# Kernel tuning notes

Hardware: AMD Instinct MI355X
Metric: run time of the kernel (lower is better)

The kernel has to match this reference:

```python
import jax, jax.numpy as jnp
import numpy as np

B, N, M, D = 4, 2048, 2048, 512
BLUR, SCALING, P = 0.05, 0.9, 2          # geomloss: blur=epsilon, p=2
DIAMETER = 2.0                            # max distance between unit-norm points
# geomloss epsilon_schedule: diameter^p annealed down to blur^p by scaling^p
_sched = np.arange(P * np.log(DIAMETER), P * np.log(BLUR), P * np.log(SCALING))
EPS_LIST = np.concatenate([[DIAMETER ** P], np.exp(_sched), [BLUR ** P]]).astype(np.float32)


def setup_inputs() -> dict:
    key = jax.random.key(0)
    k1, k2 = jax.random.split(key)
    return {
        "E_p": jax.random.normal(k1, (B, N, D), jnp.float32),
        "E_t": jax.random.normal(k2, (B, M, D), jnp.float32),
    }


def _l2norm(x):
    return x / jnp.maximum(jnp.linalg.norm(x, axis=-1, keepdims=True), 1e-12)


def _cost(x, y):
    # C(x,y) = ||x - y||^2 / 2  (geomloss squared_distances / 2 for p=2)
    x2 = jnp.sum(x * x, axis=-1)[:, :, None]   # (B, N, 1)
    y2 = jnp.sum(y * y, axis=-1)[:, None, :]   # (B, 1, M)
    return 0.5 * (x2 + y2 - 2.0 * jnp.einsum("bnd,bmd->bnm", x, y))


def _softmin(eps, C, h):
    # h: (B, M) = log_weights + potential/eps ;  returns (B, N)
    return -eps * jax.nn.logsumexp(h[:, None, :] - C / eps, axis=-1)


def _sinkhorn_divergence(x, y):
    b, n = x.shape[0], x.shape[1]
    m = y.shape[1]
    C_xy = _cost(x, y)
    C_yx = jnp.swapaxes(C_xy, 1, 2)
    C_xx = _cost(x, x)
    C_yy = _cost(y, y)
    log_a = jnp.full((b, n), -np.log(n), x.dtype)   # uniform weights
    log_b = jnp.full((b, m), -np.log(m), x.dtype)

    sg = jax.lax.stop_gradient
    Cxy_s, Cyx_s, Cxx_s, Cyy_s = sg(C_xy), sg(C_yx), sg(C_xx), sg(C_yy)

    # init at the largest epsilon (geomloss sinkhorn_loop init)
    eps0 = float(EPS_LIST[0])
    f_ba = _softmin(eps0, Cxy_s, log_b)
    g_ab = _softmin(eps0, Cyx_s, log_a)
    f_aa = _softmin(eps0, Cxx_s, log_a)
    g_bb = _softmin(eps0, Cyy_s, log_b)

    def body(carry, eps):
        f_aa, g_bb, g_ab, f_ba = carry
        ft_ba = _softmin(eps, Cxy_s, log_b + g_ab / eps)
        gt_ab = _softmin(eps, Cyx_s, log_a + f_ba / eps)
        ft_aa = _softmin(eps, Cxx_s, log_a + f_aa / eps)
        gt_bb = _softmin(eps, Cyy_s, log_b + g_bb / eps)
        new = (0.5 * (f_aa + ft_aa), 0.5 * (g_bb + gt_bb),
               0.5 * (g_ab + gt_ab), 0.5 * (f_ba + ft_ba))
        return new, None

    (f_aa, g_bb, g_ab, f_ba), _ = jax.lax.scan(
        body, (f_aa, g_bb, g_ab, f_ba), jnp.asarray(EPS_LIST))

    # last extrapolation at final eps (gradients flow through the cost only,
    # matching geomloss's detached-potential final step)
    eps = float(EPS_LIST[-1])
    f_ba_f = _softmin(eps, C_xy, sg(log_b + g_ab / eps))
    g_ab_f = _softmin(eps, C_yx, sg(log_a + f_ba / eps))
    f_aa_f = _softmin(eps, C_xx, sg(log_a + f_aa / eps))
    g_bb_f = _softmin(eps, C_yy, sg(log_b + g_bb / eps))

    a_w = jnp.exp(log_a)
    b_w = jnp.exp(log_b)
    loss = (jnp.sum(a_w * (f_ba_f - f_aa_f), axis=-1)
            + jnp.sum(b_w * (g_ab_f - g_bb_f), axis=-1))   # (B,)
    return jnp.mean(loss)


def reference(E_p, E_t):
    return _sinkhorn_divergence(_l2norm(E_p), _l2norm(E_t))
```

## Files before the change

### kernel.cpp

```cpp
#include <hip/hip_runtime.h>
#include <hip/hip_bf16.h>
#include <hip/hip_fp16.h>
#include <math.h>

#define B_ 4
#define N_ 2048
#define D_ 512

typedef __bf16    bf16x8  __attribute__((ext_vector_type(8)));
typedef float     floatx4 __attribute__((ext_vector_type(4)));
typedef _Float16  half8   __attribute__((ext_vector_type(8)));

#if __has_builtin(__builtin_amdgcn_exp2f)
__device__ __forceinline__ float fexp2(float x) { return __builtin_amdgcn_exp2f(x); }
#else
__device__ __forceinline__ float fexp2(float x) { return exp2f(x); }
#endif
#if __has_builtin(__builtin_amdgcn_logf)
__device__ __forceinline__ float flog2(float x) { return __builtin_amdgcn_logf(x); }
#else
__device__ __forceinline__ float flog2(float x) { return __log2f(x); }
#endif

__device__ __forceinline__ void gload16(const void* g, void* l) {
  __builtin_amdgcn_global_load_lds(
      (const __attribute__((address_space(1))) void*)g,
      (__attribute__((address_space(3))) void*)l, 16, 0, 0);
}

__global__ __launch_bounds__(256) void norm_kernel(const float* __restrict__ in,
                                                   __hip_bfloat16* __restrict__ out) {
  const size_t row = blockIdx.x;
  const int t = threadIdx.x;
  const float* src = in + row * D_;
  float v0 = src[t], v1 = src[t + 256];
  float ss = fmaf(v0, v0, v1 * v1);
#pragma unroll
  for (int off = 1; off < 64; off <<= 1) ss += __shfl_xor(ss, off);
  __shared__ float red[4];
  if ((t & 63) == 0) red[t >> 6] = ss;
  __syncthreads();
  const float tot = red[0] + red[1] + red[2] + red[3];
  const float scale = 1.0f / fmaxf(sqrtf(tot), 1e-12f);
  out[row * D_ + t]       = __float2bfloat16(v0 * scale);
  out[row * D_ + t + 256] = __float2bfloat16(v1 * scale);
}

__global__ __launch_bounds__(256) void gram_gemm(const __hip_bfloat16* __restrict__ X,
                                                 const __hip_bfloat16* __restrict__ Y,
                                                 __half* __restrict__ Gxy,
                                                 __half* __restrict__ Gxx,
                                                 __half* __restrict__ Gyy) {
  __shared__ __hip_bfloat16 As[128 * 32];
  __shared__ __hip_bfloat16 Bs[128 * 32];
  const int t = threadIdx.x;
  const int wave = t >> 6, lane = t & 63;
  const int bm0 = blockIdx.x * 128, bn0 = blockIdx.y * 128;
  const int mat = blockIdx.z >> 2;
  const size_t bb = blockIdx.z & 3;
  const __hip_bfloat16* Ab = (mat == 2 ? Y : X) + bb * (size_t)(N_ * D_);
  const __hip_bfloat16* Bb = (mat == 1 ? X : Y) + bb * (size_t)(N_ * D_);
  __half* Gb = (mat == 0 ? Gxy : mat == 1 ? Gxx : Gyy) + bb * (size_t)N_ * N_;

  floatx4 acc[4][4] = {};
  const int wr = wave >> 1, wc = wave & 1;
  const int srow = t >> 2;
  const int scol = (t & 3) * 8;
  char* AsB = (char*)As;
  char* BsB = (char*)Bs;
  const int ldsOff = wave * 1024;

  for (int k0 = 0; k0 < D_; k0 += 32) {
    __syncthreads();
    gload16(Ab + (size_t)(bm0 + srow)      * D_ + k0 + scol, AsB + ldsOff);
    gload16(Ab + (size_t)(bm0 + 64 + srow) * D_ + k0 + scol, AsB + 4096 + ldsOff);
    gload16(Bb + (size_t)(bn0 + srow)      * D_ + k0 + scol, BsB + ldsOff);
    gload16(Bb + (size_t)(bn0 + 64 + srow) * D_ + k0 + scol, BsB + 4096 + ldsOff);
    __syncthreads();

    const int lrow = lane & 15, lk = (lane >> 4) * 8;
    bf16x8 af[4], bfr[4];
#pragma unroll
    for (int mi = 0; mi < 4; ++mi)
      af[mi] = *(const bf16x8*)((const char*)As + ((wr * 64 + mi * 16 + lrow) * 32 + lk) * 2);
#pragma unroll
    for (int ni = 0; ni < 4; ++ni)
      bfr[ni] = *(const bf16x8*)((const char*)Bs + ((wc * 64 + ni * 16 + lrow) * 32 + lk) * 2);
#pragma unroll
    for (int mi = 0; mi < 4; ++mi)
#pragma unroll
      for (int ni = 0; ni < 4; ++ni)
        acc[mi][ni] = __builtin_amdgcn_mfma_f32_16x16x32_bf16(af[mi], bfr[ni], acc[mi][ni], 0, 0, 0);
  }

  const int orow = (lane >> 4) * 4, ocol = lane & 15;
#pragma unroll
  for (int mi = 0; mi < 4; ++mi)
#pragma unroll
    for (int ni = 0; ni < 4; ++ni) {
      const int row = bm0 + wr * 64 + mi * 16 + orow;
      const int col = bn0 + wc * 64 + ni * 16 + ocol;
#pragma unroll
      for (int r = 0; r < 4; ++r)
        Gb[(size_t)(row + r) * N_ + col] = __float2half(acc[mi][ni][r]);
    }
}

#define L2E_ 1.44269504088896f
#define LN2_ 0.69314718055995f

template <int MODE>
__global__ __launch_bounds__(256) void sink_stream(
    const __half* __restrict__ Gxy, const __half* __restrict__ Gxx,
    const __half* __restrict__ Gyy,
    const float* __restrict__ potOld, float* __restrict__ potNew,
    float2* __restrict__ colPart, float eps, float* __restrict__ out) {
  __shared__ float2 part[4][32];

  const int bid = blockIdx.x;
  const int mat = bid % 3;
  const int rem = bid / 3;
  const int b = rem >> 6, stripe = rem & 63;
  const int lane = threadIdx.x & 63, wave = threadIdx.x >> 6;
  const int c0 = wave * 512 + lane * 8;

  const float inv_eps = 1.0f / eps;
  const float ieL  = inv_eps * L2E_;
  const float hbL  = (-7.62461898616f - inv_eps) * L2E_;
  const float negEpsLn2 = -eps * LN2_;

  const __half* G = (mat == 0 ? Gxy : mat == 1 ? Gxx : Gyy) + (size_t)b * N_ * N_;
  const int hIdx = (mat == 0) ? 1 : (mat == 1) ? 2 : 3;
  const int oIdx = (mat == 0) ? 0 : hIdx;
  const float* potH = potOld + ((size_t)hIdx * B_ + b) * N_;
  const float* potR = potOld + ((size_t)0    * B_ + b) * N_;
  const float* potO = potOld + ((size_t)oIdx * B_ + b) * N_;
  float*       potW = potNew + ((size_t)oIdx * B_ + b) * N_;

  float hh[8];
  if constexpr (MODE == 0) {
#pragma unroll
    for (int e = 0; e < 8; ++e) hh[e] = hbL;
  } else {
    const float4 a = *(const float4*)(potH + c0);
    const float4 c = *(const float4*)(potH + c0 + 4);
    hh[0] = fmaf(a.x, ieL, hbL); hh[1] = fmaf(a.y, ieL, hbL);
    hh[2] = fmaf(a.z, ieL, hbL); hh[3] = fmaf(a.w, ieL, hbL);
    hh[4] = fmaf(c.x, ieL, hbL); hh[5] = fmaf(c.y, ieL, hbL);
    hh[6] = fmaf(c.z, ieL, hbL); hh[7] = fmaf(c.w, ieL, hbL);
  }

  float colm[8], cols_[8];
#pragma unroll
  for (int e = 0; e < 8; ++e) { colm[e] = -3.0e38f; cols_[e] = 0.0f; }

  const int rbase = stripe * 32;
  const __half* gbase = G + (size_t)rbase * N_ + c0;

  half8 A0, A1, P0, P1;
  A0 = *(const half8*)(gbase);
  A1 = *(const half8*)(gbase + N_);

#pragma unroll 1
  for (int it = 0; it < 16; ++it) {
    if (it < 15) {
      const __half* gp = gbase + (size_t)(it * 2 + 2) * N_;
      P0 = *(const half8*)(gp);
      P1 = *(const half8*)(gp + N_);
    }

    const int r0 = rbase + it * 2;
    float hr0 = hbL, hr1 = hbL;
    if (mat == 0 && MODE != 0) {
      hr0 = fmaf(potR[r0],     ieL, hbL);
      hr1 = fmaf(potR[r0 + 1], ieL, hbL);
    }

    float t0[8], t1[8];
    float mx0 = -3.0e38f, mx1 = -3.0e38f;
#pragma unroll
    for (int e = 0; e < 8; ++e) {
      t0[e] = fmaf((float)A0[e], ieL, hh[e]);
      t1[e] = fmaf((float)A1[e], ieL, hh[e]);
      mx0 = fmaxf(mx0, t0[e]);
      mx1 = fmaxf(mx1, t1[e]);
    }
#pragma unroll
    for (int off = 1; off < 64; off <<= 1) {
      mx0 = fmaxf(mx0, __shfl_xor(mx0, off));
      mx1 = fmaxf(mx1, __shfl_xor(mx1, off));
    }

    float sm0 = 0.0f, sm1 = 0.0f;
#pragma unroll
    for (int e = 0; e < 8; ++e) {
      sm0 += fexp2(t0[e] - mx0);
      sm1 += fexp2(t1[e] - mx1);
    }
#pragma unroll
    for (int off = 1; off < 64; off <<= 1) {
      sm0 += __shfl_xor(sm0, off);
      sm1 += __shfl_xor(sm1, off);
    }
    if (lane == 0) {
      part[wave][it * 2]     = make_float2(mx0, sm0);
      part[wave][it * 2 + 1] = make_float2(mx1, sm1);
    }

    if (mat == 0) {
      const float d0 = hr0, d1 = hr1;
#pragma unroll
      for (int e = 0; e < 8; ++e) {
        const float s0 = t0[e] - hh[e] + d0;
        const float s1 = t1[e] - hh[e] + d1;
        const float nm = fmaxf(colm[e], fmaxf(s0, s1));
        const float add = fexp2(s0 - nm) + fexp2(s1 - nm);
        cols_[e] = fmaf(cols_[e], fexp2(colm[e] - nm), add);
        colm[e] = nm;
      }
    }

    A0 = P0; A1 = P1;
  }

  if (mat == 0) {
    float2* cp = colPart + ((size_t)(b * 64 + stripe) * 2048 + c0);
#pragma unroll
    for (int e = 0; e < 8; ++e) cp[e] = make_float2(colm[e], cols_[e]);
  }

  __syncthreads();

  float vfin = 0.0f;
  if (wave == 0 && lane < 32) {
    float2 q = part[0][lane];
    float m = q.x, s = q.y;
#pragma unroll
    for (int w = 1; w < 4; ++w) {
      const float2 q2 = part[w][lane];
      const float nm = fmaxf(m, q2.x);
      s = fmaf(s, fexp2(m - nm), q2.y * fexp2(q2.x - nm));
      m = nm;
    }
    const float v = negEpsLn2 * (m + flog2(s));
    const int r = rbase + lane;
    if constexpr (MODE == 0) {
      potW[r] = v;
    } else if constexpr (MODE == 1) {
      potW[r] = 0.5f * (potO[r] + v);
    } else {
      vfin = v;
    }
  }

  if constexpr (MODE == 2) {
#pragma unroll
    for (int off = 1; off < 64; off <<= 1) vfin += __shfl_xor(vfin, off);
    if (threadIdx.x == 0) {
      const float sign = (mat == 0) ? 1.0f : -1.0f;
      atomicAdd(out, sign * vfin * (1.0f / (2048.0f * B_)));
    }
  }
}

template <int MODE>
__global__ __launch_bounds__(256) void sink_merge(
    const float2* __restrict__ colPart, const float* __restrict__ potOld,
    float* __restrict__ potNew, float eps, float* __restrict__ out) {
  __shared__ float2 mp[3][64];
  const int lane = threadIdx.x & 63, sub = threadIdx.x >> 6;
  const int colg = blockIdx.x * 64 + lane;
  const int b = colg >> 11, col = colg & 2047;
  const float negEpsLn2 = -eps * LN2_;

  float m = -3.0e38f, s = 0.0f;
  const float2* cp = colPart + ((size_t)(b * 64 + sub * 16)) * 2048 + col;
#pragma unroll
  for (int st = 0; st < 16; ++st) {
    const float2 P = cp[(size_t)st * 2048];
    const float nm = fmaxf(m, P.x);
    s = fmaf(s, fexp2(m - nm), P.y * fexp2(P.x - nm));
    m = nm;
  }
  if (sub != 0) mp[sub - 1][lane] = make_float2(m, s);
  __syncthreads();

  float vfin = 0.0f;
  if (sub == 0) {
#pragma unroll
    for (int w = 0; w < 3; ++w) {
      const float2 q = mp[w][lane];
      const float nm = fmaxf(m, q.x);
      s = fmaf(s, fexp2(m - nm), q.y * fexp2(q.x - nm));
      m = nm;
    }
    const float v = negEpsLn2 * (m + flog2(s));
    if constexpr (MODE == 0) {
      potNew[((size_t)1 * B_ + b) * N_ + col] = v;
    } else if constexpr (MODE == 1) {
      potNew[((size_t)1 * B_ + b) * N_ + col] =
          0.5f * (potOld[((size_t)1 * B_ + b) * N_ + col] + v);
    } else {
      vfin = v;
    }
  }

  if constexpr (MODE == 2) {
#pragma unroll
    for (int off = 1; off < 64; off <<= 1) vfin += __shfl_xor(vfin, off);
    __shared__ float red[4];
    if ((threadIdx.x & 63) == 0) red[sub] = vfin;
    __syncthreads();
    if (threadIdx.x == 0)
      atomicAdd(out, (red[0] + red[1] + red[2] + red[3]) * (1.0f / (2048.0f * B_)));
  }
}

extern "C" void kernel_launch(void* const* d_in, const int* in_sizes, int n_in,
                              void* d_out, int out_size, void* d_ws, size_t ws_size,
                              hipStream_t stream) {
  const float* E_p = (const float*)d_in[0];
  const float* E_t = (const float*)d_in[1];
  float* out = (float*)d_out;
  char* ws = (char*)d_ws;

  size_t off = 0;
  auto alloc = [&](size_t bytes) {
    void* p = ws + off;
    off += (bytes + 255) & ~(size_t)255;
    return p;
  };
  __hip_bfloat16* Xb = (__hip_bfloat16*)alloc((size_t)B_ * N_ * D_ * 2);
  __hip_bfloat16* Yb = (__hip_bfloat16*)alloc((size_t)B_ * N_ * D_ * 2);
  __half* Gxy = (__half*)alloc((size_t)B_ * N_ * N_ * 2);
  __half* Gxx = (__half*)alloc((size_t)B_ * N_ * N_ * 2);
  __half* Gyy = (__half*)alloc((size_t)B_ * N_ * N_ * 2);
  float* potA = (float*)alloc((size_t)4 * B_ * N_ * 4);
  float* potB = (float*)alloc((size_t)4 * B_ * N_ * 4);
  float2* colPart = (float2*)alloc((size_t)B_ * 64 * 2048 * 8);

  norm_kernel<<<B_ * N_, 256, 0, stream>>>(E_p, Xb);
  norm_kernel<<<B_ * N_, 256, 0, stream>>>(E_t, Yb);

  dim3 gg(16, 16, 12);
  gram_gemm<<<gg, 256, 0, stream>>>(Xb, Yb, Gxy, Gxx, Gyy);

  float epsl[48];
  int ne = 0;
  epsl[ne++] = 4.0f;
  {
    const double lstart = 2.0 * log(2.0);
    const double lstop  = 2.0 * log(0.05);
    const double lstep  = 2.0 * log(0.9);
    for (int k = 0;; ++k) {
      const double v = lstart + k * lstep;
      if (!(v > lstop)) break;
      epsl[ne++] = (float)exp(v);
    }
  }
  epsl[ne++] = 0.0025f;

  (void)hipMemsetAsync(d_out, 0, sizeof(float), stream);

  sink_stream<0><<<768, 256, 0, stream>>>(Gxy, Gxx, Gyy, potA, potA, colPart,
                                          epsl[0], nullptr);
  sink_merge<0><<<128, 256, 0, stream>>>(colPart, potA, potA, epsl[0], nullptr);

  float* cur = potA;
  float* nxt = potB;
  for (int i = 0; i < ne; ++i) {
    sink_stream<1><<<768, 256, 0, stream>>>(Gxy, Gxx, Gyy, cur, nxt, colPart,
                                            epsl[i], nullptr);
    sink_merge<1><<<128, 256, 0, stream>>>(colPart, cur, nxt, epsl[i], nullptr);
    float* tmp = cur; cur = nxt; nxt = tmp;
  }

  sink_stream<2><<<768, 256, 0, stream>>>(Gxy, Gxx, Gyy, cur, cur, colPart,
                                          epsl[ne - 1], out);
  sink_merge<2><<<128, 256, 0, stream>>>(colPart, cur, cur, epsl[ne - 1], out);
}
```

Before: 1.273 ms.

## Halve stripe height to double grid and process four rows per iteration

New measurement: 1.379 ms. 1.08x slower.

```diff
diff --git a/kernel.cpp b/kernel.cpp
--- a/kernel.cpp
+++ b/kernel.cpp
@@ -115,12 +115,12 @@
     const __half* __restrict__ Gyy,
     const float* __restrict__ potOld, float* __restrict__ potNew,
     float2* __restrict__ colPart, float eps, float* __restrict__ out) {
-  __shared__ float2 part[4][32];
+  __shared__ float2 part[4][16];
 
   const int bid = blockIdx.x;
   const int mat = bid % 3;
   const int rem = bid / 3;
-  const int b = rem >> 6, stripe = rem & 63;
+  const int b = rem >> 7, stripe = rem & 127;
   const int lane = threadIdx.x & 63, wave = threadIdx.x >> 6;
   const int c0 = wave * 512 + lane * 8;
 
@@ -154,77 +154,86 @@
 #pragma unroll
   for (int e = 0; e < 8; ++e) { colm[e] = -3.0e38f; cols_[e] = 0.0f; }
 
-  const int rbase = stripe * 32;
+  const int rbase = stripe * 16;
   const __half* gbase = G + (size_t)rbase * N_ + c0;
 
-  half8 A0, A1, P0, P1;
-  A0 = *(const half8*)(gbase);
-  A1 = *(const half8*)(gbase + N_);
+  half8 A[4], P[4];
+#pragma unroll
+  for (int r = 0; r < 4; ++r) A[r] = *(const half8*)(gbase + (size_t)r * N_);
 
 #pragma unroll 1
-  for (int it = 0; it < 16; ++it) {
-    if (it < 15) {
-      const __half* gp = gbase + (size_t)(it * 2 + 2) * N_;
-      P0 = *(const half8*)(gp);
-      P1 = *(const half8*)(gp + N_);
-    }
-
-    const int r0 = rbase + it * 2;
-    float hr0 = hbL, hr1 = hbL;
-    if (mat == 0 && MODE != 0) {
-      hr0 = fmaf(potR[r0],     ieL, hbL);
-      hr1 = fmaf(potR[r0 + 1], ieL, hbL);
-    }
-
-    float t0[8], t1[8];
-    float mx0 = -3.0e38f, mx1 = -3.0e38f;
-#pragma unroll
-    for (int e = 0; e < 8; ++e) {
-      t0[e] = fmaf((float)A0[e], ieL, hh[e]);
-      t1[e] = fmaf((float)A1[e], ieL, hh[e]);
-      mx0 = fmaxf(mx0, t0[e]);
-      mx1 = fmaxf(mx1, t1[e]);
+  for (int it = 0; it < 4; ++it) {
+    if (it < 3) {
+#pragma unroll
+      for (int r = 0; r < 4; ++r)
+        P[r] = *(const half8*)(gbase + (size_t)(it * 4 + 4 + r) * N_);
+    }
+
+    const int r0 = rbase + it * 4;
+    float hr[4];
+    if (mat == 0) {
+      if constexpr (MODE != 0) {
+#pragma unroll
+        for (int r = 0; r < 4; ++r) hr[r] = fmaf(potR[r0 + r], ieL, hbL);
+      } else {
+#pragma unroll
+        for (int r = 0; r < 4; ++r) hr[r] = hbL;
+      }
+    }
+
+    float mx[4];
+#pragma unroll
+    for (int r = 0; r < 4; ++r) {
+      float m = fmaf((float)A[r][0], ieL, hh[0]);
+#pragma unroll
+      for (int e = 1; e < 8; ++e) m = fmaxf(m, fmaf((float)A[r][e], ieL, hh[e]));
+      mx[r] = m;
     }
 #pragma unroll
     for (int off = 1; off < 64; off <<= 1) {
-      mx0 = fmaxf(mx0, __shfl_xor(mx0, off));
-      mx1 = fmaxf(mx1, __shfl_xor(mx1, off));
-    }
-
-    float sm0 = 0.0f, sm1 = 0.0f;
-#pragma unroll
-    for (int e = 0; e < 8; ++e) {
-      sm0 += fexp2(t0[e] - mx0);
-      sm1 += fexp2(t1[e] - mx1);
-    }
+#pragma unroll
+      for (int r = 0; r < 4; ++r) mx[r] = fmaxf(mx[r], __shfl_xor(mx[r], off));
+    }
+
+    float sm[4] = {0.0f, 0.0f, 0.0f, 0.0f};
+#pragma unroll
+    for (int r = 0; r < 4; ++r)
+#pragma unroll
+      for (int e = 0; e < 8; ++e)
+        sm[r] += fexp2(fmaf((float)A[r][e], ieL, hh[e]) - mx[r]);
 #pragma unroll
     for (int off = 1; off < 64; off <<= 1) {
-      sm0 += __shfl_xor(sm0, off);
-      sm1 += __shfl_xor(sm1, off);
-    }
+#pragma unroll
+      for (int r = 0; r < 4; ++r) sm[r] += __shfl_xor(sm[r], off);
+    }
+
     if (lane == 0) {
-      part[wave][it * 2]     = make_float2(mx0, sm0);
-      part[wave][it * 2 + 1] = make_float2(mx1, sm1);
+#pragma unroll
+      for (int r = 0; r < 4; ++r)
+        part[wave][it * 4 + r] = make_float2(mx[r], sm[r]);
     }
 
     if (mat == 0) {
-      const float d0 = hr0, d1 = hr1;
 #pragma unroll
       for (int e = 0; e < 8; ++e) {
-        const float s0 = t0[e] - hh[e] + d0;
-        const float s1 = t1[e] - hh[e] + d1;
-        const float nm = fmaxf(colm[e], fmaxf(s0, s1));
-        const float add = fexp2(s0 - nm) + fexp2(s1 - nm);
+        const float s0 = fmaf((float)A[0][e], ieL, hr[0]);
+        const float s1 = fmaf((float)A[1][e], ieL, hr[1]);
+        const float s2 = fmaf((float)A[2][e], ieL, hr[2]);
+        const float s3 = fmaf((float)A[3][e], ieL, hr[3]);
+        const float nm = fmaxf(fmaxf(fmaxf(s0, s1), fmaxf(s2, s3)), colm[e]);
+        const float add = fexp2(s0 - nm) + fexp2(s1 - nm)
+                        + fexp2(s2 - nm) + fexp2(s3 - nm);
         cols_[e] = fmaf(cols_[e], fexp2(colm[e] - nm), add);
         colm[e] = nm;
       }
     }
 
-    A0 = P0; A1 = P1;
+#pragma unroll
+    for (int r = 0; r < 4; ++r) A[r] = P[r];
   }
 
   if (mat == 0) {
-    float2* cp = colPart + ((size_t)(b * 64 + stripe) * 2048 + c0);
+    float2* cp = colPart + ((size_t)(b * 128 + stripe) * 2048 + c0);
 #pragma unroll
     for (int e = 0; e < 8; ++e) cp[e] = make_float2(colm[e], cols_[e]);
   }
@@ -232,7 +241,7 @@
   __syncthreads();
 
   float vfin = 0.0f;
-  if (wave == 0 && lane < 32) {
+  if (wave == 0 && lane < 16) {
     float2 q = part[0][lane];
     float m = q.x, s = q.y;
 #pragma unroll
@@ -274,9 +283,9 @@
   const float negEpsLn2 = -eps * LN2_;
 
   float m = -3.0e38f, s = 0.0f;
-  const float2* cp = colPart + ((size_t)(b * 64 + sub * 16)) * 2048 + col;
-#pragma unroll
-  for (int st = 0; st < 16; ++st) {
+  const float2* cp = colPart + ((size_t)(b * 128 + sub * 32)) * 2048 + col;
+#pragma unroll 8
+  for (int st = 0; st < 32; ++st) {
     const float2 P = cp[(size_t)st * 2048];
     const float nm = fmaxf(m, P.x);
     s = fmaf(s, fexp2(m - nm), P.y * fexp2(P.x - nm));
@@ -337,7 +346,7 @@
   __half* Gyy = (__half*)alloc((size_t)B_ * N_ * N_ * 2);
   float* potA = (float*)alloc((size_t)4 * B_ * N_ * 4);
   float* potB = (float*)alloc((size_t)4 * B_ * N_ * 4);
-  float2* colPart = (float2*)alloc((size_t)B_ * 64 * 2048 * 8);
+  float2* colPart = (float2*)alloc((size_t)B_ * 128 * 2048 * 8);
 
   norm_kernel<<<B_ * N_, 256, 0, stream>>>(E_p, Xb);
   norm_kernel<<<B_ * N_, 256, 0, stream>>>(E_t, Yb);
@@ -362,20 +371,20 @@
 
   (void)hipMemsetAsync(d_out, 0, sizeof(float), stream);
 
-  sink_stream<0><<<768, 256, 0, stream>>>(Gxy, Gxx, Gyy, potA, potA, colPart,
-                                          epsl[0], nullptr);
+  sink_stream<0><<<1536, 256, 0, stream>>>(Gxy, Gxx, Gyy, potA, potA, colPart,
+                                           epsl[0], nullptr);
   sink_merge<0><<<128, 256, 0, stream>>>(colPart, potA, potA, epsl[0], nullptr);
 
   float* cur = potA;
   float* nxt = potB;
   for (int i = 0; i < ne; ++i) {
-    sink_stream<1><<<768, 256, 0, stream>>>(Gxy, Gxx, Gyy, cur, nxt, colPart,
-                                            epsl[i], nullptr);
+    sink_stream<1><<<1536, 256, 0, stream>>>(Gxy, Gxx, Gyy, cur, nxt, colPart,
+                                             epsl[i], nullptr);
     sink_merge<1><<<128, 256, 0, stream>>>(colPart, cur, nxt, epsl[i], nullptr);
     float* tmp = cur; cur = nxt; nxt = tmp;
   }
 
-  sink_stream<2><<<768, 256, 0, stream>>>(Gxy, Gxx, Gyy, cur, cur, colPart,
-                                          epsl[ne - 1], out);
+  sink_stream<2><<<1536, 256, 0, stream>>>(Gxy, Gxx, Gyy, cur, cur, colPart,
+                                           epsl[ne - 1], out);
   sink_merge<2><<<128, 256, 0, stream>>>(colPart, cur, cur, epsl[ne - 1], out);
 }
```
